# Kernel optimization log

Measured on AMD Instinct MI355X. Metric: run time of the kernel, lower is better.

The kernel has to match this reference:

```python
import jax, jax.numpy as jnp
import numpy as np

EMBED_DIM = 1024
N_HEADS = 16
HEAD_DIM = EMBED_DIM // N_HEADS
EPS = 1e-6


def setup_inputs() -> dict:
    key = jax.random.key(0)
    k_x, k_wqkv, k_bqkv, k_wo, k_bo = jax.random.split(key, 5)
    B, T, C = 2, 2048, EMBED_DIM
    s = 1.0 / np.sqrt(C)
    return {
        "x": jax.random.normal(k_x, (B, T, C), dtype=jnp.float32),
        "w_qkv": jax.random.normal(k_wqkv, (C, 3 * C), dtype=jnp.float32) * s,
        "b_qkv": jax.random.normal(k_bqkv, (3 * C,), dtype=jnp.float32) * s,
        "w_out": jax.random.normal(k_wo, (C, C), dtype=jnp.float32) * s,
        "b_out": jax.random.normal(k_bo, (C,), dtype=jnp.float32) * s,
    }


def reference(x, w_qkv, b_qkv, w_out, b_out):
    B, T, C = x.shape
    H, D = N_HEADS, HEAD_DIM
    qkv = x @ w_qkv + b_qkv                       # [B,T,3C]
    q, k, v = jnp.split(qkv, 3, axis=-1)
    # [B,H,T,D]
    q = q.reshape(B, T, H, D).transpose(0, 2, 1, 3)
    k = k.reshape(B, T, H, D).transpose(0, 2, 1, 3)
    v = v.reshape(B, T, H, D).transpose(0, 2, 1, 3)
    dot = jnp.einsum("bhqd,bhkd->bhqk", q, k)     # [B,H,T,T]
    q_sq = jnp.sum(q * q, axis=-1)[..., :, None]  # [B,H,T,1]
    k_sq = jnp.sum(k * k, axis=-1)[..., None, :]  # [B,H,1,T]
    scores = (dot * dot) / (q_sq + k_sq - 2.0 * dot + EPS)
    causal = jnp.tril(jnp.ones((T, T), dtype=bool))
    scores = jnp.where(causal, scores, -jnp.inf)
    attn = jax.nn.softmax(scores, axis=-1)
    out = jnp.einsum("bhqk,bhkd->bhqd", attn, v)  # [B,H,T,D]
    out = out.transpose(0, 2, 1, 3).reshape(B, T, C)
    return out @ w_out + b_out
```

## Files before the change

### kernel.cpp

```cpp
#include <hip/hip_runtime.h>
#include <stdint.h>


#define TSEQ 2048
#define BATCH 2

typedef _Float16 f16x8 __attribute__((ext_vector_type(8)));
typedef _Float16 f16x2h __attribute__((ext_vector_type(2)));
typedef __fp16 fp16x2 __attribute__((ext_vector_type(2)));
typedef float f32x4 __attribute__((ext_vector_type(4)));
typedef unsigned int u32x2 __attribute__((ext_vector_type(2)));

#define MFMA16(a, b, c) __builtin_amdgcn_mfma_f32_16x16x32_f16(a, b, c, 0, 0, 0)

__device__ __forceinline__ unsigned short f2h(float f) {
  union { _Float16 h; unsigned short u; } v;
  v.h = (_Float16)f;
  return v.u;
}
__device__ __forceinline__ unsigned int pack2h(float lo, float hi) {
  return (unsigned int)f2h(lo) | ((unsigned int)f2h(hi) << 16);
}
__device__ __forceinline__ float dot2acc(unsigned int u, float acc) {
  union { unsigned int u; f16x2h h; } c;
  c.u = u;
  return __builtin_amdgcn_fdot2(c.h, c.h, acc, false);
}
__device__ __forceinline__ void async_ld16(const void* g, const void* l) {
  __builtin_amdgcn_global_load_lds((const __attribute__((address_space(1))) void*)g,
                                   (__attribute__((address_space(3))) void*)l,
                                   16, 0, 0);
}
__device__ __forceinline__ unsigned int pk_f16(float lo, float hi) {
  union { fp16x2 h; unsigned int u; } c;
  c.h = __builtin_amdgcn_cvt_pkrtz(lo, hi);
  return c.u;
}

__global__ __launch_bounds__(256) void prep(const float* __restrict__ x,
                                            unsigned short* __restrict__ xh,
                                            const float* __restrict__ w_qkv,
                                            unsigned short* __restrict__ wqkvT,
                                            const float* __restrict__ w_out,
                                            unsigned short* __restrict__ woT) {
  __shared__ unsigned short tile[32][33];
  const int bid = blockIdx.x, tid = threadIdx.x;
  if (bid < 2048) {
    const int i = (bid * 256 + tid) * 8;
    const float4 a = *(const float4*)(x + i);
    const float4 b = *(const float4*)(x + i + 4);
    uint4 o;
    o.x = pack2h(a.x, a.y); o.y = pack2h(a.z, a.w);
    o.z = pack2h(b.x, b.y); o.w = pack2h(b.z, b.w);
    *(uint4*)(xh + i) = o;
    return;
  }
  const bool qkv = bid < 5120;
  const int b2 = qkv ? bid - 2048 : bid - 5120;
  const int NB = qkv ? 96 : 32;
  const int N = NB * 32, K = 1024;
  const float* src = qkv ? w_qkv : w_out;
  unsigned short* dst = qkv ? wqkvT : woT;
  const int nb = (b2 % NB) * 32, kb = (b2 / NB) * 32;
  const int tx = tid & 31, ty = tid >> 5;
#pragma unroll
  for (int i = 0; i < 4; i++)
    tile[ty + 8 * i][tx] = f2h(src[(size_t)(kb + ty + 8 * i) * N + nb + tx]);
  __syncthreads();
#pragma unroll
  for (int i = 0; i < 4; i++)
    dst[(size_t)(nb + ty + 8 * i) * K + kb + tx] = tile[tx][ty + 8 * i];
}

template <int TN, bool OUT_F32>
__global__ __launch_bounds__(256) void gemm_bt(const unsigned short* __restrict__ A,
                                               const unsigned short* __restrict__ Bt,
                                               const float* __restrict__ bias,
                                               void* __restrict__ Cp,
                                               int N, int K) {
  __shared__ __attribute__((aligned(16))) unsigned short Atile[128 * 32];
  __shared__ __attribute__((aligned(16))) unsigned short Btile[TN * 32];
  constexpr int NJ = TN / 32;
  const int tid = threadIdx.x;
  const int w = tid >> 6, lane = tid & 63;
  const int quad = lane >> 4, l15 = lane & 15;
  const int m0 = blockIdx.y * 128, n0 = blockIdx.x * TN;
  const int wr = w >> 1, wc = w & 1;
  const int nwc = wc * (TN / 2);
  f32x4 acc[4][NJ] = {};
  for (int kt = 0; kt < K; kt += 32) {
    __syncthreads();
#pragma unroll
    for (int it = 0; it < 2; it++) {
      const int c = it * 256 + tid;
      async_ld16(A + (size_t)(m0 + (c >> 2)) * K + kt + (c & 3) * 8,
                 &Atile[(size_t)(it * 256 + w * 64) * 8]);
    }
#pragma unroll
    for (int it = 0; it < TN / 64; it++) {
      const int c = it * 256 + tid;
      async_ld16(Bt + (size_t)(n0 + (c >> 2)) * K + kt + (c & 3) * 8,
                 &Btile[(size_t)(it * 256 + w * 64) * 8]);
    }
    __syncthreads();
    f16x8 af[4], bfr[NJ];
#pragma unroll
    for (int i = 0; i < 4; i++)
      af[i] = *(const f16x8*)&Atile[(wr * 64 + i * 16 + l15) * 32 + quad * 8];
#pragma unroll
    for (int j = 0; j < NJ; j++)
      bfr[j] = *(const f16x8*)&Btile[(nwc + j * 16 + l15) * 32 + quad * 8];
#pragma unroll
    for (int i = 0; i < 4; i++)
#pragma unroll
      for (int j = 0; j < NJ; j++)
        acc[i][j] = MFMA16(af[i], bfr[j], acc[i][j]);
  }
#pragma unroll
  for (int j = 0; j < NJ; j++) {
    const int n = n0 + nwc + j * 16 + l15;
    const float bv = bias[n];
#pragma unroll
    for (int i = 0; i < 4; i++) {
      const int mb = m0 + wr * 64 + i * 16 + quad * 4;
#pragma unroll
      for (int r = 0; r < 4; r++) {
        if constexpr (OUT_F32)
          ((float*)Cp)[(size_t)(mb + r) * N + n] = acc[i][j][r] + bv;
        else
          ((unsigned short*)Cp)[(size_t)(mb + r) * N + n] = f2h(acc[i][j][r] + bv);
      }
    }
  }
}

__global__ __launch_bounds__(256, 4) void yat_attn(const unsigned short* __restrict__ qkv,
                                                   unsigned short* __restrict__ outp) {
  __shared__ __attribute__((aligned(16))) unsigned short Kp[2][64 * 72];
  __shared__ __attribute__((aligned(16))) unsigned short Vt[2][64 * 72];
  __shared__ float qsq[64], ksq[2][64];
  const int tid = threadIdx.x;
  const int w = tid >> 6, lane = tid & 63;
  const int quad = lane >> 4, l15 = lane & 15;
  const int bh = blockIdx.x, b = bh >> 4, h = bh & 15;
  const int y = blockIdx.y;
  const int qt = (y < 8) ? 31 - y : (y < 16) ? y - 8 : (y < 24) ? 39 - y : y - 16;
  const unsigned short* base = qkv + (size_t)b * TSEQ * 3072 + h * 64;
  const int t = tid >> 2, dc = (tid & 3) * 16;
  const int d0 = tid & 31, tg8 = tid >> 5;

  uint4 kreg0, kreg1;
  unsigned int vreg[8];
  {
    const unsigned short* gk = base + 1024 + (size_t)t * 3072 + dc;
    kreg0 = *(const uint4*)gk;
    kreg1 = *(const uint4*)(gk + 8);
    const unsigned short* gv = base + 2048 + (size_t)(tg8 * 8) * 3072 + 2 * d0;
#pragma unroll
    for (int s = 0; s < 8; s++)
      vreg[s] = *(const unsigned int*)(gv + (size_t)s * 3072);
  }
  {
    const unsigned short* g = base + (size_t)(qt * 64 + t) * 3072 + dc;
    uint4 v0 = *(const uint4*)g;
    uint4 v1 = *(const uint4*)(g + 8);
    *(uint4*)&Kp[1][t * 72 + dc] = v0;
    *(uint4*)&Kp[1][t * 72 + dc + 8] = v1;
    float s = dot2acc(v0.x, 0.f);
    s = dot2acc(v0.y, s); s = dot2acc(v0.z, s); s = dot2acc(v0.w, s);
    s = dot2acc(v1.x, s); s = dot2acc(v1.y, s); s = dot2acc(v1.z, s);
    s = dot2acc(v1.w, s);
    s += __shfl_xor(s, 1);
    s += __shfl_xor(s, 2);
    if ((tid & 3) == 0) qsq[t] = s;
  }
  auto commit = [&](int buf) {
    *(uint4*)&Kp[buf][t * 72 + dc] = kreg0;
    *(uint4*)&Kp[buf][t * 72 + dc + 8] = kreg1;
    float s = dot2acc(kreg0.x, 0.f);
    s = dot2acc(kreg0.y, s); s = dot2acc(kreg0.z, s); s = dot2acc(kreg0.w, s);
    s = dot2acc(kreg1.x, s); s = dot2acc(kreg1.y, s); s = dot2acc(kreg1.z, s);
    s = dot2acc(kreg1.w, s);
    s += __shfl_xor(s, 1);
    s += __shfl_xor(s, 2);
    if ((tid & 3) == 0) ksq[buf][t] = s;
    uint4 LO, HI;
    LO.x = __builtin_amdgcn_perm(vreg[1], vreg[0], 0x05040100u);
    HI.x = __builtin_amdgcn_perm(vreg[1], vreg[0], 0x07060302u);
    LO.y = __builtin_amdgcn_perm(vreg[3], vreg[2], 0x05040100u);
    HI.y = __builtin_amdgcn_perm(vreg[3], vreg[2], 0x07060302u);
    LO.z = __builtin_amdgcn_perm(vreg[5], vreg[4], 0x05040100u);
    HI.z = __builtin_amdgcn_perm(vreg[5], vreg[4], 0x07060302u);
    LO.w = __builtin_amdgcn_perm(vreg[7], vreg[6], 0x05040100u);
    HI.w = __builtin_amdgcn_perm(vreg[7], vreg[6], 0x07060302u);
    *(uint4*)&Vt[buf][(2 * d0) * 72 + tg8 * 8] = LO;
    *(uint4*)&Vt[buf][(2 * d0 + 1) * 72 + tg8 * 8] = HI;
  };
  commit(0);
  if (qt >= 1) {
    const unsigned short* gk = base + 1024 + (size_t)(64 + t) * 3072 + dc;
    kreg0 = *(const uint4*)gk;
    kreg1 = *(const uint4*)(gk + 8);
    const unsigned short* gv = base + 2048 + (size_t)(64 + tg8 * 8) * 3072 + 2 * d0;
#pragma unroll
    for (int s = 0; s < 8; s++)
      vreg[s] = *(const unsigned int*)(gv + (size_t)s * 3072);
  }
  __syncthreads();
  const f16x8 aq0 = *(const f16x8*)&Kp[1][(w * 16 + l15) * 72 + quad * 8];
  const f16x8 aq1 = *(const f16x8*)&Kp[1][(w * 16 + l15) * 72 + 32 + quad * 8];
  const f16x8 onesf = {(_Float16)1.f, (_Float16)1.f, (_Float16)1.f, (_Float16)1.f,
                       (_Float16)1.f, (_Float16)1.f, (_Float16)1.f, (_Float16)1.f};
  const int ql = w * 16 + l15;
  const float qsq_eps = qsq[ql] + 1e-6f;
  __syncthreads();

  f32x4 accO[4] = {};
  float m_run = 0.f;
  float l_acc = 0.f;

  for (int kt = 0; kt <= qt; kt++) {
    const int cur = kt & 1;
    f32x4 accS[4] = {};
#pragma unroll
    for (int nt = 0; nt < 4; nt++) {
      const f16x8 bk0 = *(const f16x8*)&Kp[cur][(nt * 16 + l15) * 72 + quad * 8];
      const f16x8 bk1 = *(const f16x8*)&Kp[cur][(nt * 16 + l15) * 72 + 32 + quad * 8];
      accS[nt] = MFMA16(bk0, aq0, accS[nt]);
      accS[nt] = MFMA16(bk1, aq1, accS[nt]);
    }
    f32x4 sc[4];
#pragma unroll
    for (int nt = 0; nt < 4; nt++) {
      const f32x4 k4 = *(const f32x4*)&ksq[cur][nt * 16 + quad * 4];
      const f32x4 dv = accS[nt];
      f32x4 den = (k4 + qsq_eps) + dv * -2.f;
      f32x4 rc;
      rc[0] = __builtin_amdgcn_rcpf(den[0]);
      rc[1] = __builtin_amdgcn_rcpf(den[1]);
      rc[2] = __builtin_amdgcn_rcpf(den[2]);
      rc[3] = __builtin_amdgcn_rcpf(den[3]);
      sc[nt] = dv * dv * rc;
    }
    if (kt == qt) {
#pragma unroll
      for (int nt = 0; nt < 4; nt++)
#pragma unroll
        for (int r = 0; r < 4; r++)
          if (nt * 16 + quad * 4 + r > ql) sc[nt][r] = -1e30f;
    }
    const f32x4 t01 = __builtin_elementwise_max(sc[0], sc[1]);
    const f32x4 t23 = __builtin_elementwise_max(sc[2], sc[3]);
    const f32x4 t4 = __builtin_elementwise_max(t01, t23);
    float tm = fmaxf(fmaxf(t4[0], t4[1]), fmaxf(t4[2], t4[3]));
    tm = fmaxf(tm, __shfl_xor(tm, 16));
    tm = fmaxf(tm, __shfl_xor(tm, 32));
    const float mn = fmaxf(m_run, tm);
    const float alpha = __expf(m_run - mn);
    m_run = mn;
    unsigned int pa[4], pb[4];
#pragma unroll
    for (int nt = 0; nt < 4; nt++) {
      const f32x4 e = sc[nt] - m_run;
      pa[nt] = pk_f16(__expf(e[0]), __expf(e[1]));
      pb[nt] = pk_f16(__expf(e[2]), __expf(e[3]));
    }
    if (kt < qt) commit(cur ^ 1);
    if (kt + 2 <= qt) {
      const unsigned short* gk = base + 1024 + (size_t)((kt + 2) * 64 + t) * 3072 + dc;
      kreg0 = *(const uint4*)gk;
      kreg1 = *(const uint4*)(gk + 8);
      const unsigned short* gv =
          base + 2048 + (size_t)((kt + 2) * 64 + tg8 * 8) * 3072 + 2 * d0;
#pragma unroll
      for (int s = 0; s < 8; s++)
        vreg[s] = *(const unsigned int*)(gv + (size_t)s * 3072);
    }
    union { f16x8 v; unsigned int u[4]; } bp0, bp1;
    {
      u32x2 s0 = __builtin_amdgcn_permlane32_swap(pa[0], pa[1], false, false);
      u32x2 s1 = __builtin_amdgcn_permlane16_swap(s0.x, s0.y, false, false);
      bp0.u[0] = s1.x; bp0.u[2] = s1.y;
      s0 = __builtin_amdgcn_permlane32_swap(pb[0], pb[1], false, false);
      s1 = __builtin_amdgcn_permlane16_swap(s0.x, s0.y, false, false);
      bp0.u[1] = s1.x; bp0.u[3] = s1.y;
      s0 = __builtin_amdgcn_permlane32_swap(pa[2], pa[3], false, false);
      s1 = __builtin_amdgcn_permlane16_swap(s0.x, s0.y, false, false);
      bp1.u[0] = s1.x; bp1.u[2] = s1.y;
      s0 = __builtin_amdgcn_permlane32_swap(pb[2], pb[3], false, false);
      s1 = __builtin_amdgcn_permlane16_swap(s0.x, s0.y, false, false);
      bp1.u[1] = s1.x; bp1.u[3] = s1.y;
    }
#pragma unroll
    for (int i = 0; i < 4; i++) accO[i] *= alpha;
    f32x4 accL = {};
    accL = MFMA16(onesf, bp0.v, accL);
    accL = MFMA16(onesf, bp1.v, accL);
#pragma unroll
    for (int i = 0; i < 4; i++) {
      const f16x8 av0 = *(const f16x8*)&Vt[cur][(i * 16 + l15) * 72 + quad * 8];
      const f16x8 av1 = *(const f16x8*)&Vt[cur][(i * 16 + l15) * 72 + 32 + quad * 8];
      accO[i] = MFMA16(av0, bp0.v, accO[i]);
      accO[i] = MFMA16(av1, bp1.v, accO[i]);
    }
    l_acc = l_acc * alpha + accL[0];
    __syncthreads();
  }

  const float linv = 1.0f / l_acc;
#pragma unroll
  for (int i = 0; i < 4; i++)
#pragma unroll
    for (int r = 0; r < 4; r++)
      Kp[0][(w * 16 + l15) * 72 + i * 16 + quad * 4 + r] = f2h(accO[i][r] * linv);
  __syncthreads();
  {
    uint4 o0 = *(const uint4*)&Kp[0][t * 72 + dc];
    uint4 o1 = *(const uint4*)&Kp[0][t * 72 + dc + 8];
    unsigned short* g = outp + (size_t)(b * TSEQ + qt * 64 + t) * 1024 + h * 64 + dc;
    *(uint4*)g = o0;
    *(uint4*)(g + 8) = o1;
  }
}

extern "C" void kernel_launch(void* const* d_in, const int* in_sizes, int n_in,
                              void* d_out, int out_size, void* d_ws, size_t ws_size,
                              hipStream_t stream) {
  (void)in_sizes; (void)n_in; (void)out_size; (void)ws_size;
  const float* x     = (const float*)d_in[0];
  const float* w_qkv = (const float*)d_in[1];
  const float* b_qkv = (const float*)d_in[2];
  const float* w_out = (const float*)d_in[3];
  const float* b_out = (const float*)d_in[4];
  float* out = (float*)d_out;

  unsigned short* wqkvT  = (unsigned short*)d_ws;
  unsigned short* woT    = wqkvT + (size_t)3072 * 1024;
  unsigned short* qkvws  = woT + (size_t)1024 * 1024;
  unsigned short* xh     = qkvws + (size_t)4096 * 3072;
  unsigned short* attnws = xh;

  prep<<<dim3(6144), 256, 0, stream>>>(x, xh, w_qkv, wqkvT, w_out, woT);
  gemm_bt<128, false><<<dim3(3072 / 128, 4096 / 128), 256, 0, stream>>>(xh, wqkvT, b_qkv, qkvws, 3072, 1024);
  yat_attn<<<dim3(BATCH * 16, 32), 256, 0, stream>>>(qkvws, attnws);
  gemm_bt<64, true><<<dim3(1024 / 64, 4096 / 128), 256, 0, stream>>>(attnws, woT, b_out, out, 1024, 1024);
}
```

Measured before the change: 188.1 us.

## Software-pipeline QK^T MFMA one tile ahead of softmax in causal attention loop

Restructures the key-tile loop so the QK^T MFMAs for tile kt+1 are issued right after that tile is committed to LDS, before the softmax and PV work of tile kt. The loop is unrolled by two with ping-pong score register arrays, and the LDS commit plus a barrier move to the top of each iteration. The aim is to hide MFMA latency behind the exp, reciprocal and permlane ALU work. In exchange it adds a second barrier per iteration and more live score registers. It also drops the barrier after the Q fragment load, so the first commit into Kp[1] may race with other waves still reading Q from that buffer.

```diff
diff --git a/kernel.cpp b/kernel.cpp
--- a/kernel.cpp
+++ b/kernel.cpp
@@ -213,27 +213,40 @@
                        (_Float16)1.f, (_Float16)1.f, (_Float16)1.f, (_Float16)1.f};
   const int ql = w * 16 + l15;
   const float qsq_eps = qsq[ql] + 1e-6f;
-  __syncthreads();
 
   f32x4 accO[4] = {};
   float m_run = 0.f;
   float l_acc = 0.f;
 
-  for (int kt = 0; kt <= qt; kt++) {
-    const int cur = kt & 1;
-    f32x4 accS[4] = {};
+  f32x4 SA[4], SB[4];
+#pragma unroll
+  for (int nt = 0; nt < 4; nt++) {
+    const f16x8 bk0 = *(const f16x8*)&Kp[0][(nt * 16 + l15) * 72 + quad * 8];
+    const f16x8 bk1 = *(const f16x8*)&Kp[0][(nt * 16 + l15) * 72 + 32 + quad * 8];
+    SA[nt] = {};
+    SA[nt] = MFMA16(bk0, aq0, SA[nt]);
+    SA[nt] = MFMA16(bk1, aq1, SA[nt]);
+  }
+
+  auto body = [&](int kt, f32x4 (&Scur)[4], f32x4 (&Snext)[4], bool issue_next) {
+    const int pcur = kt & 1, pnxt = (kt + 1) & 1;
+    if (kt < qt) commit(pnxt);
+    __syncthreads();
+    if (issue_next) {
+#pragma unroll
+      for (int nt = 0; nt < 4; nt++) {
+        const f16x8 bk0 = *(const f16x8*)&Kp[pnxt][(nt * 16 + l15) * 72 + quad * 8];
+        const f16x8 bk1 = *(const f16x8*)&Kp[pnxt][(nt * 16 + l15) * 72 + 32 + quad * 8];
+        Snext[nt] = {};
+        Snext[nt] = MFMA16(bk0, aq0, Snext[nt]);
+        Snext[nt] = MFMA16(bk1, aq1, Snext[nt]);
+      }
+    }
+    f32x4 sc[4];
 #pragma unroll
     for (int nt = 0; nt < 4; nt++) {
-      const f16x8 bk0 = *(const f16x8*)&Kp[cur][(nt * 16 + l15) * 72 + quad * 8];
-      const f16x8 bk1 = *(const f16x8*)&Kp[cur][(nt * 16 + l15) * 72 + 32 + quad * 8];
-      accS[nt] = MFMA16(bk0, aq0, accS[nt]);
-      accS[nt] = MFMA16(bk1, aq1, accS[nt]);
-    }
-    f32x4 sc[4];
-#pragma unroll
-    for (int nt = 0; nt < 4; nt++) {
-      const f32x4 k4 = *(const f32x4*)&ksq[cur][nt * 16 + quad * 4];
-      const f32x4 dv = accS[nt];
+      const f32x4 k4 = *(const f32x4*)&ksq[pcur][nt * 16 + quad * 4];
+      const f32x4 dv = Scur[nt];
       f32x4 den = (k4 + qsq_eps) + dv * -2.f;
       f32x4 rc;
       rc[0] = __builtin_amdgcn_rcpf(den[0]);
@@ -265,7 +278,6 @@
       pa[nt] = pk_f16(__expf(e[0]), __expf(e[1]));
       pb[nt] = pk_f16(__expf(e[2]), __expf(e[3]));
     }
-    if (kt < qt) commit(cur ^ 1);
     if (kt + 2 <= qt) {
       const unsigned short* gk = base + 1024 + (size_t)((kt + 2) * 64 + t) * 3072 + dc;
       kreg0 = *(const uint4*)gk;
@@ -298,13 +310,22 @@
     accL = MFMA16(onesf, bp1.v, accL);
 #pragma unroll
     for (int i = 0; i < 4; i++) {
-      const f16x8 av0 = *(const f16x8*)&Vt[cur][(i * 16 + l15) * 72 + quad * 8];
-      const f16x8 av1 = *(const f16x8*)&Vt[cur][(i * 16 + l15) * 72 + 32 + quad * 8];
+      const f16x8 av0 = *(const f16x8*)&Vt[pcur][(i * 16 + l15) * 72 + quad * 8];
+      const f16x8 av1 = *(const f16x8*)&Vt[pcur][(i * 16 + l15) * 72 + 32 + quad * 8];
       accO[i] = MFMA16(av0, bp0.v, accO[i]);
       accO[i] = MFMA16(av1, bp1.v, accO[i]);
     }
     l_acc = l_acc * alpha + accL[0];
     __syncthreads();
+  };
+
+  {
+    int kt = 0;
+    for (; kt + 1 <= qt; kt += 2) {
+      body(kt, SA, SB, true);
+      body(kt + 1, SB, SA, kt + 2 <= qt);
+    }
+    if (kt <= qt) body(kt, SA, SB, false);
   }
 
   const float linv = 1.0f / l_acc;
```

After: 196.7 us. +4.6%, slower.

## Use 128-row query tiles with 8 waves sharing each K/V tile in attention

Applied to the files above, without the earlier changes.

The attention kernel now processes 128 query rows per block with 512 threads (8 waves), so each loaded 64-row K/V tile is reused by twice as many query rows and the global K/V traffic per query is halved. The grid drops to 16 blocks per head, the causal mask covers the last two key tiles, and query and output staging borrow the second K/V shared buffers. In exchange the grid is half the size and the causal work is coarser, so each block does some extra masked work and per-CU occupancy may change.

```diff
diff --git a/kernel.cpp b/kernel.cpp
--- a/kernel.cpp
+++ b/kernel.cpp
@@ -134,38 +134,41 @@
   }
 }
 
-__global__ __launch_bounds__(256, 4) void yat_attn(const unsigned short* __restrict__ qkv,
-                                                   unsigned short* __restrict__ outp) {
+__global__ __launch_bounds__(512) void yat_attn(const unsigned short* __restrict__ qkv,
+                                                unsigned short* __restrict__ outp) {
   __shared__ __attribute__((aligned(16))) unsigned short Kp[2][64 * 72];
   __shared__ __attribute__((aligned(16))) unsigned short Vt[2][64 * 72];
-  __shared__ float qsq[64], ksq[2][64];
+  __shared__ float qsq[128], ksq[2][64];
   const int tid = threadIdx.x;
   const int w = tid >> 6, lane = tid & 63;
   const int quad = lane >> 4, l15 = lane & 15;
   const int bh = blockIdx.x, b = bh >> 4, h = bh & 15;
   const int y = blockIdx.y;
-  const int qt = (y < 8) ? 31 - y : (y < 16) ? y - 8 : (y < 24) ? 39 - y : y - 16;
+  const int yp = (y < 8) ? 15 - y : y - 8;
+  const int NT = 2 * yp + 2;
+  const int q0 = yp * 128;
   const unsigned short* base = qkv + (size_t)b * TSEQ * 3072 + h * 64;
-  const int t = tid >> 2, dc = (tid & 3) * 16;
-  const int d0 = tid & 31, tg8 = tid >> 5;
-
-  uint4 kreg0, kreg1;
-  unsigned int vreg[8];
+  const int t = tid >> 2, dcq = (tid & 3) * 16;
+  const int tk = tid >> 3, dk = (tid & 7) * 8;
+  const int d0 = tid & 31, tg = tid >> 5;
+
+  uint4 kreg;
+  unsigned int vreg[4];
   {
-    const unsigned short* gk = base + 1024 + (size_t)t * 3072 + dc;
-    kreg0 = *(const uint4*)gk;
-    kreg1 = *(const uint4*)(gk + 8);
-    const unsigned short* gv = base + 2048 + (size_t)(tg8 * 8) * 3072 + 2 * d0;
-#pragma unroll
-    for (int s = 0; s < 8; s++)
+    const unsigned short* gk = base + 1024 + (size_t)tk * 3072 + dk;
+    kreg = *(const uint4*)gk;
+    const unsigned short* gv = base + 2048 + (size_t)(tg * 4) * 3072 + 2 * d0;
+#pragma unroll
+    for (int s = 0; s < 4; s++)
       vreg[s] = *(const unsigned int*)(gv + (size_t)s * 3072);
   }
   {
-    const unsigned short* g = base + (size_t)(qt * 64 + t) * 3072 + dc;
+    const unsigned short* g = base + (size_t)(q0 + t) * 3072 + dcq;
     uint4 v0 = *(const uint4*)g;
     uint4 v1 = *(const uint4*)(g + 8);
-    *(uint4*)&Kp[1][t * 72 + dc] = v0;
-    *(uint4*)&Kp[1][t * 72 + dc + 8] = v1;
+    unsigned short* qd = (t < 64) ? &Kp[1][t * 72 + dcq] : &Vt[1][(t - 64) * 72 + dcq];
+    *(uint4*)qd = v0;
+    *(uint4*)(qd + 8) = v1;
     float s = dot2acc(v0.x, 0.f);
     s = dot2acc(v0.y, s); s = dot2acc(v0.z, s); s = dot2acc(v0.w, s);
     s = dot2acc(v1.x, s); s = dot2acc(v1.y, s); s = dot2acc(v1.z, s);
@@ -175,51 +178,46 @@
     if ((tid & 3) == 0) qsq[t] = s;
   }
   auto commit = [&](int buf) {
-    *(uint4*)&Kp[buf][t * 72 + dc] = kreg0;
-    *(uint4*)&Kp[buf][t * 72 + dc + 8] = kreg1;
-    float s = dot2acc(kreg0.x, 0.f);
-    s = dot2acc(kreg0.y, s); s = dot2acc(kreg0.z, s); s = dot2acc(kreg0.w, s);
-    s = dot2acc(kreg1.x, s); s = dot2acc(kreg1.y, s); s = dot2acc(kreg1.z, s);
-    s = dot2acc(kreg1.w, s);
+    *(uint4*)&Kp[buf][tk * 72 + dk] = kreg;
+    float s = dot2acc(kreg.x, 0.f);
+    s = dot2acc(kreg.y, s); s = dot2acc(kreg.z, s); s = dot2acc(kreg.w, s);
     s += __shfl_xor(s, 1);
     s += __shfl_xor(s, 2);
-    if ((tid & 3) == 0) ksq[buf][t] = s;
-    uint4 LO, HI;
+    s += __shfl_xor(s, 4);
+    if ((tid & 7) == 0) ksq[buf][tk] = s;
+    u32x2 LO, HI;
     LO.x = __builtin_amdgcn_perm(vreg[1], vreg[0], 0x05040100u);
     HI.x = __builtin_amdgcn_perm(vreg[1], vreg[0], 0x07060302u);
     LO.y = __builtin_amdgcn_perm(vreg[3], vreg[2], 0x05040100u);
     HI.y = __builtin_amdgcn_perm(vreg[3], vreg[2], 0x07060302u);
-    LO.z = __builtin_amdgcn_perm(vreg[5], vreg[4], 0x05040100u);
-    HI.z = __builtin_amdgcn_perm(vreg[5], vreg[4], 0x07060302u);
-    LO.w = __builtin_amdgcn_perm(vreg[7], vreg[6], 0x05040100u);
-    HI.w = __builtin_amdgcn_perm(vreg[7], vreg[6], 0x07060302u);
-    *(uint4*)&Vt[buf][(2 * d0) * 72 + tg8 * 8] = LO;
-    *(uint4*)&Vt[buf][(2 * d0 + 1) * 72 + tg8 * 8] = HI;
+    *(u32x2*)&Vt[buf][(2 * d0) * 72 + tg * 4] = LO;
+    *(u32x2*)&Vt[buf][(2 * d0 + 1) * 72 + tg * 4] = HI;
   };
   commit(0);
-  if (qt >= 1) {
-    const unsigned short* gk = base + 1024 + (size_t)(64 + t) * 3072 + dc;
-    kreg0 = *(const uint4*)gk;
-    kreg1 = *(const uint4*)(gk + 8);
-    const unsigned short* gv = base + 2048 + (size_t)(64 + tg8 * 8) * 3072 + 2 * d0;
-#pragma unroll
-    for (int s = 0; s < 8; s++)
+  {
+    const unsigned short* gk = base + 1024 + (size_t)(64 + tk) * 3072 + dk;
+    kreg = *(const uint4*)gk;
+    const unsigned short* gv = base + 2048 + (size_t)(64 + tg * 4) * 3072 + 2 * d0;
+#pragma unroll
+    for (int s = 0; s < 4; s++)
       vreg[s] = *(const unsigned int*)(gv + (size_t)s * 3072);
   }
   __syncthreads();
-  const f16x8 aq0 = *(const f16x8*)&Kp[1][(w * 16 + l15) * 72 + quad * 8];
-  const f16x8 aq1 = *(const f16x8*)&Kp[1][(w * 16 + l15) * 72 + 32 + quad * 8];
+  const unsigned short* qsrc =
+      (w < 4) ? &Kp[1][(w * 16 + l15) * 72] : &Vt[1][((w - 4) * 16 + l15) * 72];
+  const f16x8 aq0 = *(const f16x8*)(qsrc + quad * 8);
+  const f16x8 aq1 = *(const f16x8*)(qsrc + 32 + quad * 8);
   const f16x8 onesf = {(_Float16)1.f, (_Float16)1.f, (_Float16)1.f, (_Float16)1.f,
                        (_Float16)1.f, (_Float16)1.f, (_Float16)1.f, (_Float16)1.f};
-  const int ql = w * 16 + l15;
-  const float qsq_eps = qsq[ql] + 1e-6f;
+  const int qrow = w * 16 + l15;
+  const float qsq_eps = qsq[qrow] + 1e-6f;
   __syncthreads();
 
   f32x4 accO[4] = {};
   float m_run = 0.f;
   float l_acc = 0.f;
 
-  for (int kt = 0; kt <= qt; kt++) {
+  for (int kt = 0; kt < NT; kt++) {
     const int cur = kt & 1;
     f32x4 accS[4] = {};
 #pragma unroll
@@ -242,12 +240,13 @@
       rc[3] = __builtin_amdgcn_rcpf(den[3]);
       sc[nt] = dv * dv * rc;
     }
-    if (kt == qt) {
+    if (kt >= NT - 2) {
+      const int koff = kt * 64 - q0 + 0;
 #pragma unroll
       for (int nt = 0; nt < 4; nt++)
 #pragma unroll
         for (int r = 0; r < 4; r++)
-          if (nt * 16 + quad * 4 + r > ql) sc[nt][r] = -1e30f;
+          if (koff + nt * 16 + quad * 4 + r > qrow) sc[nt][r] = -1e30f;
     }
     const f32x4 t01 = __builtin_elementwise_max(sc[0], sc[1]);
     const f32x4 t23 = __builtin_elementwise_max(sc[2], sc[3]);
@@ -265,15 +264,14 @@
       pa[nt] = pk_f16(__expf(e[0]), __expf(e[1]));
       pb[nt] = pk_f16(__expf(e[2]), __expf(e[3]));
     }
-    if (kt < qt) commit(cur ^ 1);
-    if (kt + 2 <= qt) {
-      const unsigned short* gk = base + 1024 + (size_t)((kt + 2) * 64 + t) * 3072 + dc;
-      kreg0 = *(const uint4*)gk;
-      kreg1 = *(const uint4*)(gk + 8);
+    if (kt + 1 < NT) commit(cur ^ 1);
+    if (kt + 2 < NT) {
+      const unsigned short* gk = base + 1024 + (size_t)((kt + 2) * 64 + tk) * 3072 + dk;
+      kreg = *(const uint4*)gk;
       const unsigned short* gv =
-          base + 2048 + (size_t)((kt + 2) * 64 + tg8 * 8) * 3072 + 2 * d0;
-#pragma unroll
-      for (int s = 0; s < 8; s++)
+          base + 2048 + (size_t)((kt + 2) * 64 + tg * 4) * 3072 + 2 * d0;
+#pragma unroll
+      for (int s = 0; s < 4; s++)
         vreg[s] = *(const unsigned int*)(gv + (size_t)s * 3072);
     }
     union { f16x8 v; unsigned int u[4]; } bp0, bp1;
@@ -308,16 +306,19 @@
   }
 
   const float linv = 1.0f / l_acc;
+  unsigned short* od =
+      (w < 4) ? &Kp[0][(w * 16 + l15) * 72] : &Vt[0][((w - 4) * 16 + l15) * 72];
 #pragma unroll
   for (int i = 0; i < 4; i++)
 #pragma unroll
     for (int r = 0; r < 4; r++)
-      Kp[0][(w * 16 + l15) * 72 + i * 16 + quad * 4 + r] = f2h(accO[i][r] * linv);
+      od[i * 16 + quad * 4 + r] = f2h(accO[i][r] * linv);
   __syncthreads();
   {
-    uint4 o0 = *(const uint4*)&Kp[0][t * 72 + dc];
-    uint4 o1 = *(const uint4*)&Kp[0][t * 72 + dc + 8];
-    unsigned short* g = outp + (size_t)(b * TSEQ + qt * 64 + t) * 1024 + h * 64 + dc;
+    const unsigned short* os = (t < 64) ? &Kp[0][t * 72] : &Vt[0][(t - 64) * 72];
+    uint4 o0 = *(const uint4*)(os + dcq);
+    uint4 o1 = *(const uint4*)(os + dcq + 8);
+    unsigned short* g = outp + (size_t)(b * TSEQ + q0 + t) * 1024 + h * 64 + dcq;
     *(uint4*)g = o0;
     *(uint4*)(g + 8) = o1;
   }
@@ -342,6 +343,6 @@
 
   prep<<<dim3(6144), 256, 0, stream>>>(x, xh, w_qkv, wqkvT, w_out, woT);
   gemm_bt<128, false><<<dim3(3072 / 128, 4096 / 128), 256, 0, stream>>>(xh, wqkvT, b_qkv, qkvws, 3072, 1024);
-  yat_attn<<<dim3(BATCH * 16, 32), 256, 0, stream>>>(qkvws, attnws);
+  yat_attn<<<dim3(BATCH * 16, 16), 512, 0, stream>>>(qkvws, attnws);
   gemm_bt<64, true><<<dim3(1024 / 64, 4096 / 128), 256, 0, stream>>>(attnws, woT, b_out, out, 1024, 1024);
 }
```

After: 194.7 us. 1.03x slower.
